# Kernel optimization log

Hardware: AMD Instinct MI355X
Metric: run time of the kernel (lower is better)

## Reference

```python
import jax, jax.numpy as jnp
import numpy as np

N_ATOMS, N_UND, N_DIR, N_ANG, N_STRUCT = 8192, 65536, 131072, 262144, 128
FEA, NRAD, NANGB, NCONV = 64, 9, 9, 4

FLOAT_NAMES = ["bond_bases_ag", "bond_bases_bg", "angle_bases", "atom_emb", "Wb", "Wa",
               "Wbw_ag", "Wbw_bg",
               "ac_cw1", "ac_cb1", "ac_cw2", "ac_cb2", "ac_gw1", "ac_gb1", "ac_gw2", "ac_gb2", "ac_out",
               "bc_cw1", "bc_cb1", "bc_cw2", "bc_cb2", "bc_gw1", "bc_gb1", "bc_gw2", "bc_gb2", "bc_out",
               "an_cw", "an_cb", "an_gw", "an_gb",
               "ro_w1", "ro_b1", "ro_w2", "ro_b2", "ro_w3", "ro_b3"]
INT_NAMES = ["atomic_numbers", "atom_graph", "directed2undirected",
             "bond_graph_atoms", "bond_graph_bonds", "atom_owners"]


def _silu(x):
    return x * jax.nn.sigmoid(x)


def _gmlp(x, cw1, cb1, cw2, cb2, gw1, gb1, gw2, gb2):
    # GatedMLP (norm=None): silu(MLP_core(x)) * sigmoid(MLP_gate(x)), each MLP = Lin-silu-Lin
    core = _silu(_silu(x @ cw1 + cb1) @ cw2 + cb2)
    gate = jax.nn.sigmoid(_silu(x @ gw1 + gb1) @ gw2 + gb2)
    return core * gate


def _forward(F, I):
    seg = jax.ops.segment_sum
    atom = F["atom_emb"][I["atomic_numbers"]]            # [N, 64]
    bond = F["bond_bases_ag"] @ F["Wb"]                  # [U, 64]
    angle = F["angle_bases"] @ F["Wa"]                   # [A, 64]
    bw_ag = F["bond_bases_ag"] @ F["Wbw_ag"]             # [U, 64]
    bw_bg = F["bond_bases_bg"] @ F["Wbw_bg"]             # [U, 64]
    ag0, ag1 = I["atom_graph"][:, 0], I["atom_graph"][:, 1]
    d2u = I["directed2undirected"]
    bgi, bgj = I["bond_graph_bonds"][:, 0], I["bond_graph_bonds"][:, 1]
    bga = I["bond_graph_atoms"]

    def atom_conv(i, atom, bond):
        msg = jnp.concatenate([atom[ag0], bond[d2u], atom[ag1]], axis=1)   # [E, 192]
        msg = _gmlp(msg, F["ac_cw1"][i], F["ac_cb1"][i], F["ac_cw2"][i], F["ac_cb2"][i],
                    F["ac_gw1"][i], F["ac_gb1"][i], F["ac_gw2"][i], F["ac_gb2"][i])
        msg = msg * bw_ag[d2u]
        # scatter-add to center atoms, linear mlp_out (no bias), resnet
        return atom + seg(msg, ag0, num_segments=N_ATOMS) @ F["ac_out"][i]

    for i in range(NCONV - 1):
        atom = atom_conv(i, atom, bond)
        # BondConv over bond graph (angles)
        tot = jnp.concatenate([bond[bgi], bond[bgj], angle, atom[bga]], axis=1)  # [A, 256]
        upd = _gmlp(tot, F["bc_cw1"][i], F["bc_cb1"][i], F["bc_cw2"][i], F["bc_cb2"][i],
                    F["bc_gw1"][i], F["bc_gb1"][i], F["bc_gw2"][i], F["bc_gb2"][i])
        upd = upd * bw_bg[bgi]
        bond = bond + seg(upd, bgi, num_segments=N_UND) @ F["bc_out"][i]
        # AngleUpdate (hidden_dim=0 -> single linear in each gated branch), resnet
        tot2 = jnp.concatenate([bond[bgi], bond[bgj], angle, atom[bga]], axis=1)
        angle = angle + _silu(tot2 @ F["an_cw"][i] + F["an_cb"][i]) * \
            jax.nn.sigmoid(tot2 @ F["an_gw"][i] + F["an_gb"][i])
    atom = atom_conv(NCONV - 1, atom, bond)

    # mlp_first readout: per-atom energy MLP then average pooling per structure
    e = _silu(atom @ F["ro_w1"] + F["ro_b1"])
    e = _silu(e @ F["ro_w2"] + F["ro_b2"])
    e = (e @ F["ro_w3"] + F["ro_b3"])[:, 0]              # [N]
    owners = I["atom_owners"]
    esum = seg(e, owners, num_segments=N_STRUCT)
    cnt = seg(jnp.ones_like(e), owners, num_segments=N_STRUCT)
    return esum / jnp.maximum(cnt, 1.0)                  # [N_STRUCT] energy/atom


def setup_inputs() -> dict:
    key = jax.random.key(0)
    ks = iter(jax.random.split(key, 64))

    def nrm(shape, fan_in):
        return jax.random.normal(next(ks), shape, dtype=jnp.float32) / np.float32(np.sqrt(fan_in))

    z = lambda *s: jnp.zeros(s, dtype=jnp.float32)
    inp = {}
    inp["atomic_numbers"] = jax.random.randint(next(ks), (N_ATOMS,), 0, 94, dtype=jnp.int32)
    inp["bond_bases_ag"] = jax.random.uniform(next(ks), (N_UND, NRAD), dtype=jnp.float32)
    inp["bond_bases_bg"] = jax.random.uniform(next(ks), (N_UND, NRAD), dtype=jnp.float32)
    inp["angle_bases"] = jax.random.uniform(next(ks), (N_ANG, NANGB), dtype=jnp.float32)
    inp["atom_graph"] = jax.random.randint(next(ks), (N_DIR, 2), 0, N_ATOMS, dtype=jnp.int32)
    inp["directed2undirected"] = jax.random.randint(next(ks), (N_DIR,), 0, N_UND, dtype=jnp.int32)
    inp["bond_graph_atoms"] = jax.random.randint(next(ks), (N_ANG,), 0, N_ATOMS, dtype=jnp.int32)
    inp["bond_graph_bonds"] = jax.random.randint(next(ks), (N_ANG, 2), 0, N_UND, dtype=jnp.int32)
    inp["atom_owners"] = jnp.sort(jax.random.randint(next(ks), (N_ATOMS,), 0, N_STRUCT, dtype=jnp.int32))
    inp["atom_emb"] = nrm((95, FEA), 1.0)
    inp["Wb"] = nrm((NRAD, FEA), NRAD)
    inp["Wa"] = nrm((NANGB, FEA), NANGB)
    inp["Wbw_ag"] = nrm((NRAD, FEA), NRAD)
    inp["Wbw_bg"] = nrm((NRAD, FEA), NRAD)
    d_a, d_b = 3 * FEA, 4 * FEA
    nb = NCONV - 1
    inp["ac_cw1"] = nrm((NCONV, d_a, FEA), d_a); inp["ac_cb1"] = z(NCONV, FEA)
    inp["ac_cw2"] = nrm((NCONV, FEA, FEA), FEA); inp["ac_cb2"] = z(NCONV, FEA)
    inp["ac_gw1"] = nrm((NCONV, d_a, FEA), d_a); inp["ac_gb1"] = z(NCONV, FEA)
    inp["ac_gw2"] = nrm((NCONV, FEA, FEA), FEA); inp["ac_gb2"] = z(NCONV, FEA)
    inp["ac_out"] = nrm((NCONV, FEA, FEA), FEA)
    inp["bc_cw1"] = nrm((nb, d_b, FEA), d_b); inp["bc_cb1"] = z(nb, FEA)
    inp["bc_cw2"] = nrm((nb, FEA, FEA), FEA); inp["bc_cb2"] = z(nb, FEA)
    inp["bc_gw1"] = nrm((nb, d_b, FEA), d_b); inp["bc_gb1"] = z(nb, FEA)
    inp["bc_gw2"] = nrm((nb, FEA, FEA), FEA); inp["bc_gb2"] = z(nb, FEA)
    inp["bc_out"] = nrm((nb, FEA, FEA), FEA)
    inp["an_cw"] = nrm((nb, d_b, FEA), d_b); inp["an_cb"] = z(nb, FEA)
    inp["an_gw"] = nrm((nb, d_b, FEA), d_b); inp["an_gb"] = z(nb, FEA)
    inp["ro_w1"] = nrm((FEA, FEA), FEA); inp["ro_b1"] = z(FEA)
    inp["ro_w2"] = nrm((FEA, FEA), FEA); inp["ro_b2"] = z(FEA)
    inp["ro_w3"] = nrm((FEA, 1), FEA); inp["ro_b3"] = z(1)
    return inp


def reference(atomic_numbers, bond_bases_ag, bond_bases_bg, angle_bases, atom_graph,
              directed2undirected, bond_graph_atoms, bond_graph_bonds, atom_owners,
              atom_emb, Wb, Wa, Wbw_ag, Wbw_bg,
              ac_cw1, ac_cb1, ac_cw2, ac_cb2, ac_gw1, ac_gb1, ac_gw2, ac_gb2, ac_out,
              bc_cw1, bc_cb1, bc_cw2, bc_cb2, bc_gw1, bc_gb1, bc_gw2, bc_gb2, bc_out,
              an_cw, an_cb, an_gw, an_gb,
              ro_w1, ro_b1, ro_w2, ro_b2, ro_w3, ro_b3):
    loc = locals()
    F = {k: loc[k] for k in FLOAT_NAMES}
    I = {k: loc[k] for k in INT_NAMES}
    return _forward(F, I)
```

## Files before the change

kernel.cpp:

```cpp
#include <hip/hip_runtime.h>
#include <hip/hip_bf16.h>

typedef float f32x4 __attribute__((ext_vector_type(4)));
typedef short s16x8 __attribute__((ext_vector_type(8)));
typedef unsigned int u32x4 __attribute__((ext_vector_type(4)));

#define DEV static __device__ __forceinline__

DEV unsigned short f2bf(float x){
    unsigned u = __builtin_bit_cast(unsigned, x);
    u += 0x7FFFu + ((u >> 16) & 1u);
    return (unsigned short)(u >> 16);
}
DEV float bf2f(unsigned short h){
    unsigned u = ((unsigned)h) << 16;
    return __builtin_bit_cast(float, u);
}
DEV float sigm_(float x){ return __builtin_amdgcn_rcpf(1.0f + __expf(-x)); }
DEV float silu_(float x){ return x * sigm_(x); }

DEV int xcd_swz(){
    int bid = blockIdx.x, nwg = gridDim.x;
    return (bid & 7) * (nwg >> 3) + (bid >> 3);
}

__global__ __launch_bounds__(256) void k_transconv(const float* __restrict__ src,
                                                   unsigned short* __restrict__ dst,
                                                   int K, int total){
    int gid = blockIdx.x * 256 + threadIdx.x;
    if (gid >= total) return;
    int kn  = K * 64;
    int b   = gid / kn;
    int rem = gid - b * kn;
    int k   = rem >> 6, n = rem & 63;
    dst[b * kn + n * K + k] = f2bf(src[gid]);
}

__global__ __launch_bounds__(256) void k_embed(const float* __restrict__ emb,
                                               const int* __restrict__ z,
                                               unsigned short* __restrict__ out){
    int gid = blockIdx.x * 256 + threadIdx.x;
    int n = gid >> 6, f = gid & 63;
    out[gid] = f2bf(emb[z[n] * 64 + f]);
}

__global__ __launch_bounds__(256) void k_smallmm(const float* __restrict__ bases,
                                                 const float* __restrict__ W,
                                                 unsigned short* __restrict__ out){
    int gid = blockIdx.x * 256 + threadIdx.x;
    int r = gid >> 6, f = gid & 63;
    const float* b = bases + r * 9;
    float acc = 0.f;
    #pragma unroll
    for (int k = 0; k < 9; ++k) acc += b[k] * W[k * 64 + f];
    out[gid] = f2bf(acc);
}

__global__ __launch_bounds__(256) void k_smallmm_perm(const float* __restrict__ bases,
                                                      const float* __restrict__ W,
                                                      const int* __restrict__ perm,
                                                      unsigned short* __restrict__ out){
    int gid = blockIdx.x * 256 + threadIdx.x;
    int r = gid >> 6, f = gid & 63;
    const float* b = bases + (size_t)perm[r] * 9;
    float acc = 0.f;
    #pragma unroll
    for (int k = 0; k < 9; ++k) acc += b[k] * W[k * 64 + f];
    out[gid] = f2bf(acc);
}

__global__ void k_count(const int* __restrict__ dst, int stride, int n, int* __restrict__ cnt){
    int i = blockIdx.x * 256 + threadIdx.x;
    if (i < n) atomicAdd(&cnt[dst[(size_t)i * stride]], 1);
}

__global__ __launch_bounds__(256) void k_bsum(const int* __restrict__ cnt,
                                              int* __restrict__ bsum){
    int i = blockIdx.x * 256 + threadIdx.x;
    int v = cnt[i];
    #pragma unroll
    for (int off = 32; off > 0; off >>= 1) v += __shfl_down(v, off);
    __shared__ int ws[4];
    if ((threadIdx.x & 63) == 0) ws[threadIdx.x >> 6] = v;
    __syncthreads();
    if (threadIdx.x == 0) bsum[blockIdx.x] = ws[0] + ws[1] + ws[2] + ws[3];
}

__global__ __launch_bounds__(256) void k_bscan(const int* __restrict__ bsum,
                                               int* __restrict__ bbase, int nb,
                                               int* __restrict__ total_out){
    __shared__ int sh[256];
    int t = threadIdx.x;
    int v = (t < nb) ? bsum[t] : 0;
    sh[t] = v;
    __syncthreads();
    for (int d = 1; d < 256; d <<= 1){
        int u = (t >= d) ? sh[t - d] : 0;
        __syncthreads();
        sh[t] += u;
        __syncthreads();
    }
    if (t < nb) bbase[t] = sh[t] - v;
    if (t == nb - 1) *total_out = sh[t];
}

__global__ __launch_bounds__(256) void k_offs(const int* __restrict__ cnt,
                                              const int* __restrict__ bbase,
                                              int* __restrict__ offs){
    __shared__ int sh[256];
    int t = threadIdx.x;
    int i = blockIdx.x * 256 + t;
    int v = cnt[i];
    sh[t] = v;
    __syncthreads();
    for (int d = 1; d < 256; d <<= 1){
        int u = (t >= d) ? sh[t - d] : 0;
        __syncthreads();
        sh[t] += u;
        __syncthreads();
    }
    offs[i] = bbase[blockIdx.x] + sh[t] - v;
}

__global__ void k_fill(const int* __restrict__ dst, int stride, int n,
                       const int* __restrict__ offs, int* __restrict__ cur,
                       int* __restrict__ idx){
    int i = blockIdx.x * 256 + threadIdx.x;
    if (i < n){
        int d = dst[(size_t)i * stride];
        int p = offs[d] + atomicAdd(&cur[d], 1);
        idx[p] = i;
    }
}

__global__ __launch_bounds__(256) void k_reduce(const unsigned short* __restrict__ upd,
                                                const int* __restrict__ offs,
                                                unsigned short* __restrict__ act, int nRows){
    int gid = blockIdx.x * 256 + threadIdx.x;
    int row = gid >> 3;
    if (row >= nRows) return;
    int c8 = (gid & 7) * 8;
    int o = offs[row], e = offs[row + 1];
    float acc[8] = {};
    for (int j = o; j < e; ++j){
        s16x8 v = *(const s16x8*)&upd[(size_t)j * 64 + c8];
        #pragma unroll
        for (int q = 0; q < 8; ++q) acc[q] += bf2f((unsigned short)v[q]);
    }
    s16x8 a = *(s16x8*)&act[(size_t)row * 64 + c8];
    #pragma unroll
    for (int q = 0; q < 8; ++q) a[q] = (short)f2bf(bf2f((unsigned short)a[q]) + acc[q]);
    *(s16x8*)&act[(size_t)row * 64 + c8] = a;
}

#define MFMA16(a,b,c) __builtin_amdgcn_mfma_f32_16x16x32_bf16(a,b,c,0,0,0)

DEV void atom_body(unsigned short* smem, int* ldsSrc, int bid,
    const unsigned short* atomBf, const unsigned short* bondBf,
    const unsigned short* bwagBf,
    const int* agraph, const int* d2u, const int* idxA,
    const unsigned short* w1cT, const unsigned short* w1gT,
    const unsigned short* w2cT, const unsigned short* w2gT,
    const unsigned short* woT,
    const float* cb1, const float* cb2, const float* gb1, const float* gb2,
    unsigned short* upd)
{
    unsigned short* ldsA  = smem;
    unsigned short* ldsHC = smem;
    unsigned short* ldsHG = smem + 4736;
    unsigned short* ldsV  = smem + 9472;
    unsigned short* ldsBw = smem + 14208;
    const int tid = threadIdx.x;
    const int r0  = bid * 64;

    {
        int q = tid >> 6, row = tid & 63;
        int e = idxA[r0 + row];
        int s;
        if (q == 0)      s = agraph[2 * e];
        else if (q == 1) s = d2u[e];
        else if (q == 2) s = agraph[2 * e + 1];
        else             s = d2u[e];
        ldsSrc[tid] = s;
    }
    __syncthreads();
    {
        const int lane8 = tid & 7;
        #pragma unroll
        for (int p = 0; p < 8; ++p){
            int cc = p * 32 + (tid >> 3);
            int q = cc >> 6, row = cc & 63;
            int s = ldsSrc[cc];
            const unsigned short* buf = (q == 1 || q == 3) ? bondBf : atomBf;
            if (q == 3) buf = bwagBf;
            u32x4 v = *(const u32x4*)(buf + (size_t)s * 64 + lane8 * 8);
            if (q < 3) *(u32x4*)&ldsA[row * 200 + q * 64 + lane8 * 8] = v;
            else       *(u32x4*)&ldsBw[row * 68 + lane8 * 8] = v;
        }
    }
    __syncthreads();

    const int lane = tid & 63;
    const int r16  = lane & 15;
    const int grp  = lane >> 4;
    const int col  = (tid >> 6) * 16 + r16;

    f32x4 aC[4] = {}, aG[4] = {};
    #pragma unroll
    for (int kt = 0; kt < 6; ++kt){
        s16x8 bc = *(const s16x8*)&w1cT[col * 192 + kt * 32 + grp * 8];
        s16x8 bg = *(const s16x8*)&w1gT[col * 192 + kt * 32 + grp * 8];
        #pragma unroll
        for (int mt = 0; mt < 4; ++mt){
            s16x8 a = *(const s16x8*)&ldsA[(mt * 16 + r16) * 200 + kt * 32 + grp * 8];
            aC[mt] = MFMA16(a, bc, aC[mt]);
            aG[mt] = MFMA16(a, bg, aG[mt]);
        }
    }
    __syncthreads();

    const float bC1 = cb1[col], bG1 = gb1[col];
    #pragma unroll
    for (int mt = 0; mt < 4; ++mt){
        #pragma unroll
        for (int j = 0; j < 4; ++j){
            int row = mt * 16 + grp * 4 + j;
            ldsHC[row * 74 + col] = f2bf(silu_(aC[mt][j] + bC1));
            ldsHG[row * 74 + col] = f2bf(silu_(aG[mt][j] + bG1));
        }
    }
    __syncthreads();

    f32x4 oC[4] = {}, oG[4] = {};
    #pragma unroll
    for (int kt = 0; kt < 2; ++kt){
        s16x8 bc = *(const s16x8*)&w2cT[col * 64 + kt * 32 + grp * 8];
        s16x8 bg = *(const s16x8*)&w2gT[col * 64 + kt * 32 + grp * 8];
        #pragma unroll
        for (int mt = 0; mt < 4; ++mt){
            s16x8 hc = *(const s16x8*)&ldsHC[(mt * 16 + r16) * 74 + kt * 32 + grp * 8];
            s16x8 hg = *(const s16x8*)&ldsHG[(mt * 16 + r16) * 74 + kt * 32 + grp * 8];
            oC[mt] = MFMA16(hc, bc, oC[mt]);
            oG[mt] = MFMA16(hg, bg, oG[mt]);
        }
    }
    const float bC2 = cb2[col], bG2 = gb2[col];
    #pragma unroll
    for (int mt = 0; mt < 4; ++mt){
        #pragma unroll
        for (int j = 0; j < 4; ++j){
            int row = mt * 16 + grp * 4 + j;
            float v = silu_(oC[mt][j] + bC2) * sigm_(oG[mt][j] + bG2);
            v *= bf2f(ldsBw[row * 68 + col]);
            ldsV[row * 74 + col] = f2bf(v);
        }
    }
    __syncthreads();

    f32x4 oD[4] = {};
    #pragma unroll
    for (int kt = 0; kt < 2; ++kt){
        s16x8 bo = *(const s16x8*)&woT[col * 64 + kt * 32 + grp * 8];
        #pragma unroll
        for (int mt = 0; mt < 4; ++mt){
            s16x8 a = *(const s16x8*)&ldsV[(mt * 16 + r16) * 74 + kt * 32 + grp * 8];
            oD[mt] = MFMA16(a, bo, oD[mt]);
        }
    }
    #pragma unroll
    for (int mt = 0; mt < 4; ++mt){
        #pragma unroll
        for (int j = 0; j < 4; ++j){
            int row = mt * 16 + grp * 4 + j;
            upd[(size_t)(r0 + row) * 64 + col] = f2bf(oD[mt][j]);
        }
    }
}

DEV void angle_body(unsigned short* ldsA, int* ldsSrc, int bid,
    const unsigned short* atomBf, const unsigned short* bondBf,
    unsigned short* angleS,
    const int* bga, const int* bgb, const int* idxB,
    const unsigned short* wcT, const unsigned short* wgT,
    const float* cb, const float* gb)
{
    const int tid = threadIdx.x;
    const int r0  = bid * 64;

    {
        int q = tid >> 6, row = tid & 63;
        int s;
        if (q == 2) s = r0 + row;
        else {
            int a = idxB[r0 + row];
            if (q == 0)      s = bgb[2 * a];
            else if (q == 1) s = bgb[2 * a + 1];
            else             s = bga[a];
        }
        ldsSrc[tid] = s;
    }
    __syncthreads();
    {
        const int lane8 = tid & 7;
        #pragma unroll
        for (int p = 0; p < 8; ++p){
            int cc = p * 32 + (tid >> 3);
            int q = cc >> 6, row = cc & 63;
            int s = ldsSrc[cc];
            const unsigned short* buf = (q < 2) ? bondBf : (q == 2 ? angleS : atomBf);
            u32x4 v = *(const u32x4*)(buf + (size_t)s * 64 + lane8 * 8);
            *(u32x4*)&ldsA[row * 264 + q * 64 + lane8 * 8] = v;
        }
    }
    __syncthreads();

    const int lane = tid & 63;
    const int r16  = lane & 15;
    const int grp  = lane >> 4;
    const int col  = (tid >> 6) * 16 + r16;

    f32x4 aC[4] = {}, aG[4] = {};
    #pragma unroll
    for (int kt = 0; kt < 8; ++kt){
        s16x8 bc = *(const s16x8*)&wcT[col * 256 + kt * 32 + grp * 8];
        s16x8 bg = *(const s16x8*)&wgT[col * 256 + kt * 32 + grp * 8];
        #pragma unroll
        for (int mt = 0; mt < 4; ++mt){
            s16x8 a = *(const s16x8*)&ldsA[(mt * 16 + r16) * 264 + kt * 32 + grp * 8];
            aC[mt] = MFMA16(a, bc, aC[mt]);
            aG[mt] = MFMA16(a, bg, aG[mt]);
        }
    }
    const float bC = cb[col], bG = gb[col];
    #pragma unroll
    for (int mt = 0; mt < 4; ++mt){
        #pragma unroll
        for (int j = 0; j < 4; ++j){
            int row = mt * 16 + grp * 4 + j;
            float oldv = bf2f(ldsA[row * 264 + 128 + col]);
            float v = silu_(aC[mt][j] + bC) * sigm_(aG[mt][j] + bG);
            angleS[(size_t)(r0 + row) * 64 + col] = f2bf(oldv + v);
        }
    }
}

__global__ __launch_bounds__(256, 4) void k_atom_conv(
    const unsigned short* __restrict__ atomBf, const unsigned short* __restrict__ bondBf,
    const unsigned short* __restrict__ bwagBf,
    const int* __restrict__ agraph, const int* __restrict__ d2u,
    const int* __restrict__ idxA,
    const unsigned short* __restrict__ w1cT, const unsigned short* __restrict__ w1gT,
    const unsigned short* __restrict__ w2cT, const unsigned short* __restrict__ w2gT,
    const unsigned short* __restrict__ woT,
    const float* __restrict__ cb1, const float* __restrict__ cb2,
    const float* __restrict__ gb1, const float* __restrict__ gb2,
    unsigned short* __restrict__ upd)
{
    __shared__ __align__(16) unsigned short smem[18560];
    __shared__ int ldsSrc[256];
    atom_body(smem, ldsSrc, xcd_swz(),
              atomBf, bondBf, bwagBf, agraph, d2u, idxA,
              w1cT, w1gT, w2cT, w2gT, woT, cb1, cb2, gb1, gb2, upd);
}

__global__ __launch_bounds__(256, 4) void k_angle_atom(
    const unsigned short* __restrict__ atomBf, const unsigned short* __restrict__ bondBf,
    unsigned short* __restrict__ angleS, const unsigned short* __restrict__ bwagBf,
    const int* __restrict__ agraph, const int* __restrict__ d2u, const int* __restrict__ idxA,
    const int* __restrict__ bga, const int* __restrict__ bgb, const int* __restrict__ idxB,
    const unsigned short* __restrict__ an_wcT, const unsigned short* __restrict__ an_wgT,
    const float* __restrict__ an_cb, const float* __restrict__ an_gb,
    const unsigned short* __restrict__ ac_w1cT, const unsigned short* __restrict__ ac_w1gT,
    const unsigned short* __restrict__ ac_w2cT, const unsigned short* __restrict__ ac_w2gT,
    const unsigned short* __restrict__ ac_woT,
    const float* __restrict__ ac_cb1, const float* __restrict__ ac_cb2,
    const float* __restrict__ ac_gb1, const float* __restrict__ ac_gb2,
    unsigned short* __restrict__ upd, int nbAngle)
{
    __shared__ __align__(16) unsigned short smem[18560];
    __shared__ int ldsSrc[256];
    int bid = blockIdx.x;
    if (bid < nbAngle){
        angle_body(smem, ldsSrc, bid, atomBf, bondBf, angleS, bga, bgb, idxB,
                   an_wcT, an_wgT, an_cb, an_gb);
    } else {
        atom_body(smem, ldsSrc, bid - nbAngle,
                  atomBf, bondBf, bwagBf, agraph, d2u, idxA,
                  ac_w1cT, ac_w1gT, ac_w2cT, ac_w2gT, ac_woT,
                  ac_cb1, ac_cb2, ac_gb1, ac_gb2, upd);
    }
}

__global__ __launch_bounds__(256, 4) void k_bond_conv(
    const unsigned short* __restrict__ atomBf, const unsigned short* __restrict__ bondBf,
    const unsigned short* __restrict__ angleS, const unsigned short* __restrict__ bwbgBf,
    const int* __restrict__ bga, const int* __restrict__ bgb,
    const int* __restrict__ idxB,
    const unsigned short* __restrict__ w1cT, const unsigned short* __restrict__ w1gT,
    const unsigned short* __restrict__ w2cT, const unsigned short* __restrict__ w2gT,
    const unsigned short* __restrict__ woT,
    const float* __restrict__ cb1, const float* __restrict__ cb2,
    const float* __restrict__ gb1, const float* __restrict__ gb2,
    unsigned short* __restrict__ upd)
{
    __shared__ __align__(16) unsigned short lds[16896];
    __shared__ int ldsSrc[256];
    unsigned short* ldsA  = lds;
    unsigned short* ldsHC = lds;
    unsigned short* ldsHG = lds + 4736;
    unsigned short* ldsV  = lds + 9472;
    const int tid = threadIdx.x;
    const int r0  = xcd_swz() * 64;

    {
        int q = tid >> 6, row = tid & 63;
        int s;
        if (q == 2) s = r0 + row;
        else {
            int a = idxB[r0 + row];
            if (q == 0)      s = bgb[2 * a];
            else if (q == 1) s = bgb[2 * a + 1];
            else             s = bga[a];
        }
        ldsSrc[tid] = s;
    }
    __syncthreads();
    {
        const int lane8 = tid & 7;
        #pragma unroll
        for (int p = 0; p < 8; ++p){
            int cc = p * 32 + (tid >> 3);
            int q = cc >> 6, row = cc & 63;
            int s = ldsSrc[cc];
            const unsigned short* buf = (q < 2) ? bondBf : (q == 2 ? angleS : atomBf);
            u32x4 v = *(const u32x4*)(buf + (size_t)s * 64 + lane8 * 8);
            *(u32x4*)&ldsA[row * 264 + q * 64 + lane8 * 8] = v;
        }
    }
    __syncthreads();

    const int lane = tid & 63;
    const int r16  = lane & 15;
    const int grp  = lane >> 4;
    const int col  = (tid >> 6) * 16 + r16;

    unsigned short bwv[16];
    #pragma unroll
    for (int mt = 0; mt < 4; ++mt)
        #pragma unroll
        for (int j = 0; j < 4; ++j)
            bwv[mt * 4 + j] = bwbgBf[(size_t)ldsSrc[mt * 16 + grp * 4 + j] * 64 + col];

    f32x4 aC[4] = {}, aG[4] = {};
    #pragma unroll
    for (int kt = 0; kt < 8; ++kt){
        s16x8 bc = *(const s16x8*)&w1cT[col * 256 + kt * 32 + grp * 8];
        s16x8 bg = *(const s16x8*)&w1gT[col * 256 + kt * 32 + grp * 8];
        #pragma unroll
        for (int mt = 0; mt < 4; ++mt){
            s16x8 a = *(const s16x8*)&ldsA[(mt * 16 + r16) * 264 + kt * 32 + grp * 8];
            aC[mt] = MFMA16(a, bc, aC[mt]);
            aG[mt] = MFMA16(a, bg, aG[mt]);
        }
    }
    __syncthreads();

    const float bC1 = cb1[col], bG1 = gb1[col];
    #pragma unroll
    for (int mt = 0; mt < 4; ++mt){
        #pragma unroll
        for (int j = 0; j < 4; ++j){
            int row = mt * 16 + grp * 4 + j;
            ldsHC[row * 74 + col] = f2bf(silu_(aC[mt][j] + bC1));
            ldsHG[row * 74 + col] = f2bf(silu_(aG[mt][j] + bG1));
        }
    }
    __syncthreads();

    f32x4 oC[4] = {}, oG[4] = {};
    #pragma unroll
    for (int kt = 0; kt < 2; ++kt){
        s16x8 bc = *(const s16x8*)&w2cT[col * 64 + kt * 32 + grp * 8];
        s16x8 bg = *(const s16x8*)&w2gT[col * 64 + kt * 32 + grp * 8];
        #pragma unroll
        for (int mt = 0; mt < 4; ++mt){
            s16x8 hc = *(const s16x8*)&ldsHC[(mt * 16 + r16) * 74 + kt * 32 + grp * 8];
            s16x8 hg = *(const s16x8*)&ldsHG[(mt * 16 + r16) * 74 + kt * 32 + grp * 8];
            oC[mt] = MFMA16(hc, bc, oC[mt]);
            oG[mt] = MFMA16(hg, bg, oG[mt]);
        }
    }
    const float bC2 = cb2[col], bG2 = gb2[col];
    #pragma unroll
    for (int mt = 0; mt < 4; ++mt){
        #pragma unroll
        for (int j = 0; j < 4; ++j){
            int row = mt * 16 + grp * 4 + j;
            float v = silu_(oC[mt][j] + bC2) * sigm_(oG[mt][j] + bG2);
            v *= bf2f(bwv[mt * 4 + j]);
            ldsV[row * 74 + col] = f2bf(v);
        }
    }
    __syncthreads();

    f32x4 oD[4] = {};
    #pragma unroll
    for (int kt = 0; kt < 2; ++kt){
        s16x8 bo = *(const s16x8*)&woT[col * 64 + kt * 32 + grp * 8];
        #pragma unroll
        for (int mt = 0; mt < 4; ++mt){
            s16x8 a = *(const s16x8*)&ldsV[(mt * 16 + r16) * 74 + kt * 32 + grp * 8];
            oD[mt] = MFMA16(a, bo, oD[mt]);
        }
    }
    #pragma unroll
    for (int mt = 0; mt < 4; ++mt){
        #pragma unroll
        for (int j = 0; j < 4; ++j){
            int row = mt * 16 + grp * 4 + j;
            upd[(size_t)(r0 + row) * 64 + col] = f2bf(oD[mt][j]);
        }
    }
}

__global__ __launch_bounds__(256) void k_readout(
    const unsigned short* __restrict__ atomBf, const int* __restrict__ owners,
    const float* __restrict__ w1, const float* __restrict__ b1,
    const float* __restrict__ w2, const float* __restrict__ b2,
    const float* __restrict__ w3, const float* __restrict__ b3,
    float* __restrict__ esum, float* __restrict__ cnt)
{
    int gid  = blockIdx.x * 256 + threadIdx.x;
    int n    = gid >> 6;
    int lane = threadIdx.x & 63;
    float a = bf2f(atomBf[n * 64 + lane]);
    float acc = b1[lane];
    #pragma unroll
    for (int k = 0; k < 64; ++k) acc += __shfl(a, k) * w1[k * 64 + lane];
    float h = silu_(acc);
    acc = b2[lane];
    #pragma unroll
    for (int k = 0; k < 64; ++k) acc += __shfl(h, k) * w2[k * 64 + lane];
    h = silu_(acc);
    float p = h * w3[lane];
    #pragma unroll
    for (int off = 32; off > 0; off >>= 1) p += __shfl_xor(p, off);
    if (lane == 0){
        atomicAdd(&esum[owners[n]], p + b3[0]);
        atomicAdd(&cnt[owners[n]], 1.0f);
    }
}

__global__ void k_final(const float* __restrict__ esum, const float* __restrict__ cnt,
                        float* __restrict__ out){
    int i = threadIdx.x;
    if (i < 128) out[i] = esum[i] / fmaxf(cnt[i], 1.0f);
}

extern "C" void kernel_launch(void* const* d_in, const int* in_sizes, int n_in,
                              void* d_out, int out_size, void* d_ws, size_t ws_size,
                              hipStream_t stream)
{
    (void)in_sizes; (void)n_in; (void)out_size; (void)ws_size;
    const int N_ATOMS = 8192, N_UND = 65536, N_DIR = 131072, N_ANG = 262144;

    const int*   atomic_numbers = (const int*)  d_in[0];
    const float* bb_ag  = (const float*)d_in[1];
    const float* bb_bg  = (const float*)d_in[2];
    const float* ang_b  = (const float*)d_in[3];
    const int*   agraph = (const int*)  d_in[4];
    const int*   d2u    = (const int*)  d_in[5];
    const int*   bga    = (const int*)  d_in[6];
    const int*   bgb    = (const int*)  d_in[7];
    const int*   owners = (const int*)  d_in[8];
    const float* emb    = (const float*)d_in[9];
    const float* Wb     = (const float*)d_in[10];
    const float* Wa     = (const float*)d_in[11];
    const float* Wbwag  = (const float*)d_in[12];
    const float* Wbwbg  = (const float*)d_in[13];
    const float* ac_cw1 = (const float*)d_in[14];
    const float* ac_cb1 = (const float*)d_in[15];
    const float* ac_cw2 = (const float*)d_in[16];
    const float* ac_cb2 = (const float*)d_in[17];
    const float* ac_gw1 = (const float*)d_in[18];
    const float* ac_gb1 = (const float*)d_in[19];
    const float* ac_gw2 = (const float*)d_in[20];
    const float* ac_gb2 = (const float*)d_in[21];
    const float* ac_out = (const float*)d_in[22];
    const float* bc_cw1 = (const float*)d_in[23];
    const float* bc_cb1 = (const float*)d_in[24];
    const float* bc_cw2 = (const float*)d_in[25];
    const float* bc_cb2 = (const float*)d_in[26];
    const float* bc_gw1 = (const float*)d_in[27];
    const float* bc_gb1 = (const float*)d_in[28];
    const float* bc_gw2 = (const float*)d_in[29];
    const float* bc_gb2 = (const float*)d_in[30];
    const float* bc_out = (const float*)d_in[31];
    const float* an_cw  = (const float*)d_in[32];
    const float* an_cb  = (const float*)d_in[33];
    const float* an_gw  = (const float*)d_in[34];
    const float* an_gb  = (const float*)d_in[35];
    const float* ro_w1  = (const float*)d_in[36];
    const float* ro_b1  = (const float*)d_in[37];
    const float* ro_w2  = (const float*)d_in[38];
    const float* ro_b2  = (const float*)d_in[39];
    const float* ro_w3  = (const float*)d_in[40];
    const float* ro_b3  = (const float*)d_in[41];

    char* ws = (char*)d_ws;
    size_t off = 0;
    auto alloc = [&](size_t bytes) -> void* {
        void* p = ws + off;
        off = (off + bytes + 255) & ~(size_t)255;
        return p;
    };
    unsigned short* atomBf  = (unsigned short*)alloc((size_t)N_ATOMS * 64 * 2);
    unsigned short* bondBf  = (unsigned short*)alloc((size_t)N_UND   * 64 * 2);
    unsigned short* angleS  = (unsigned short*)alloc((size_t)N_ANG   * 64 * 2);
    unsigned short* bwagBf  = (unsigned short*)alloc((size_t)N_UND   * 64 * 2);
    unsigned short* bwbgBf  = (unsigned short*)alloc((size_t)N_UND   * 64 * 2);
    unsigned short* updBuf  = (unsigned short*)alloc((size_t)N_ANG   * 64 * 2);
    float* esum   = (float*)alloc(128 * 4);
    float* cnt    = (float*)alloc(128 * 4);
    int* offsA = (int*)alloc((N_ATOMS + 1) * 4);
    int* curA  = (int*)alloc(N_ATOMS * 4);
    int* idxA  = (int*)alloc((size_t)N_DIR * 4);
    int* offsB = (int*)alloc((N_UND + 1) * 4);
    int* curB  = (int*)alloc(N_UND * 4);
    int* idxB  = (int*)alloc((size_t)N_ANG * 4);
    int* bsum  = (int*)alloc(256 * 4);
    int* bbase = (int*)alloc(256 * 4);
    unsigned short* acw1cT = (unsigned short*)alloc((size_t)4 * 64 * 192 * 2);
    unsigned short* acw1gT = (unsigned short*)alloc((size_t)4 * 64 * 192 * 2);
    unsigned short* acw2cT = (unsigned short*)alloc((size_t)4 * 64 * 64 * 2);
    unsigned short* acw2gT = (unsigned short*)alloc((size_t)4 * 64 * 64 * 2);
    unsigned short* acoT   = (unsigned short*)alloc((size_t)4 * 64 * 64 * 2);
    unsigned short* bcw1cT = (unsigned short*)alloc((size_t)3 * 64 * 256 * 2);
    unsigned short* bcw1gT = (unsigned short*)alloc((size_t)3 * 64 * 256 * 2);
    unsigned short* bcw2cT = (unsigned short*)alloc((size_t)3 * 64 * 64 * 2);
    unsigned short* bcw2gT = (unsigned short*)alloc((size_t)3 * 64 * 64 * 2);
    unsigned short* bcoT   = (unsigned short*)alloc((size_t)3 * 64 * 64 * 2);
    unsigned short* anwcT  = (unsigned short*)alloc((size_t)3 * 64 * 256 * 2);
    unsigned short* anwgT  = (unsigned short*)alloc((size_t)3 * 64 * 256 * 2);

    hipMemsetAsync(curA, 0, N_ATOMS * 4, stream);
    k_count<<<(N_DIR + 255) / 256, 256, 0, stream>>>(agraph, 2, N_DIR, curA);
    k_bsum <<<N_ATOMS / 256, 256, 0, stream>>>(curA, bsum);
    k_bscan<<<1, 256, 0, stream>>>(bsum, bbase, N_ATOMS / 256, offsA + N_ATOMS);
    k_offs <<<N_ATOMS / 256, 256, 0, stream>>>(curA, bbase, offsA);
    hipMemsetAsync(curA, 0, N_ATOMS * 4, stream);
    k_fill<<<(N_DIR + 255) / 256, 256, 0, stream>>>(agraph, 2, N_DIR, offsA, curA, idxA);

    hipMemsetAsync(curB, 0, N_UND * 4, stream);
    k_count<<<(N_ANG + 255) / 256, 256, 0, stream>>>(bgb, 2, N_ANG, curB);
    k_bsum <<<N_UND / 256, 256, 0, stream>>>(curB, bsum);
    k_bscan<<<1, 256, 0, stream>>>(bsum, bbase, N_UND / 256, offsB + N_UND);
    k_offs <<<N_UND / 256, 256, 0, stream>>>(curB, bbase, offsB);
    hipMemsetAsync(curB, 0, N_UND * 4, stream);
    k_fill<<<(N_ANG + 255) / 256, 256, 0, stream>>>(bgb, 2, N_ANG, offsB, curB, idxB);

    auto tc = [&](const float* src, unsigned short* dst, int B, int K){
        int total = B * K * 64;
        k_transconv<<<(total + 255) / 256, 256, 0, stream>>>(src, dst, K, total);
    };
    tc(ac_cw1, acw1cT, 4, 192);  tc(ac_gw1, acw1gT, 4, 192);
    tc(ac_cw2, acw2cT, 4, 64);   tc(ac_gw2, acw2gT, 4, 64);
    tc(ac_out, acoT,   4, 64);
    tc(bc_cw1, bcw1cT, 3, 256);  tc(bc_gw1, bcw1gT, 3, 256);
    tc(bc_cw2, bcw2cT, 3, 64);   tc(bc_gw2, bcw2gT, 3, 64);
    tc(bc_out, bcoT,   3, 64);
    tc(an_cw,  anwcT,  3, 256);  tc(an_gw,  anwgT,  3, 256);

    k_embed<<<N_ATOMS * 64 / 256, 256, 0, stream>>>(emb, atomic_numbers, atomBf);
    k_smallmm<<<N_UND * 64 / 256, 256, 0, stream>>>(bb_ag, Wb,    bondBf);
    k_smallmm_perm<<<N_ANG * 64 / 256, 256, 0, stream>>>(ang_b, Wa, idxB, angleS);
    k_smallmm<<<N_UND * 64 / 256, 256, 0, stream>>>(bb_ag, Wbwag, bwagBf);
    k_smallmm<<<N_UND * 64 / 256, 256, 0, stream>>>(bb_bg, Wbwbg, bwbgBf);

    k_atom_conv<<<N_DIR / 64, 256, 0, stream>>>(
        atomBf, bondBf, bwagBf, agraph, d2u, idxA,
        acw1cT, acw1gT, acw2cT, acw2gT, acoT,
        ac_cb1, ac_cb2, ac_gb1, ac_gb2, updBuf);
    k_reduce<<<N_ATOMS * 8 / 256, 256, 0, stream>>>(updBuf, offsA, atomBf, N_ATOMS);

    const int NB_AN = N_ANG / 64;
    const int NB_AC = N_DIR / 64;
    for (int i = 0; i < 3; ++i){
        k_bond_conv<<<NB_AN, 256, 0, stream>>>(
            atomBf, bondBf, angleS, bwbgBf, bga, bgb, idxB,
            bcw1cT + (size_t)i * 64 * 256, bcw1gT + (size_t)i * 64 * 256,
            bcw2cT + (size_t)i * 64 * 64,  bcw2gT + (size_t)i * 64 * 64,
            bcoT   + (size_t)i * 64 * 64,
            bc_cb1 + i * 64, bc_cb2 + i * 64, bc_gb1 + i * 64, bc_gb2 + i * 64, updBuf);
        k_reduce<<<N_UND * 8 / 256, 256, 0, stream>>>(updBuf, offsB, bondBf, N_UND);
        k_angle_atom<<<NB_AN + NB_AC, 256, 0, stream>>>(
            atomBf, bondBf, angleS, bwagBf,
            agraph, d2u, idxA, bga, bgb, idxB,
            anwcT + (size_t)i * 64 * 256, anwgT + (size_t)i * 64 * 256,
            an_cb + i * 64, an_gb + i * 64,
            acw1cT + (size_t)(i + 1) * 64 * 192, acw1gT + (size_t)(i + 1) * 64 * 192,
            acw2cT + (size_t)(i + 1) * 64 * 64,  acw2gT + (size_t)(i + 1) * 64 * 64,
            acoT   + (size_t)(i + 1) * 64 * 64,
            ac_cb1 + (i + 1) * 64, ac_cb2 + (i + 1) * 64,
            ac_gb1 + (i + 1) * 64, ac_gb2 + (i + 1) * 64,
            updBuf, NB_AN);
        k_reduce<<<N_ATOMS * 8 / 256, 256, 0, stream>>>(updBuf, offsA, atomBf, N_ATOMS);
    }

    hipMemsetAsync(esum, 0, 128 * 4, stream);
    hipMemsetAsync(cnt,  0, 128 * 4, stream);
    k_readout<<<N_ATOMS * 64 / 256, 256, 0, stream>>>(
        atomBf, owners, ro_w1, ro_b1, ro_w2, ro_b2, ro_w3, ro_b3, esum, cnt);
    k_final<<<1, 128, 0, stream>>>(esum, cnt, (float*)d_out);
}
```

Baseline: 859.4 us.

## Precompute sorted gather index tables and merge small setup kernels

Adds setup kernels that build per-row int4 tables of gather sources (srcA, srcB) once. The conv kernels then read their source indices straight from these tables instead of doing double-indirect lookups through idxA/idxB, and the ldsSrc staging with its barrier is removed. The three small basis matmuls are fused into one kernel, and paired weight transposes now share launches, which cuts launch count. The cost is extra index-table memory, about 6 MB, and uncoalesced strided global index reads inside the gather loop.

```diff
diff --git a/kernel.cpp b/kernel.cpp
--- a/kernel.cpp
+++ b/kernel.cpp
@@ -36,6 +36,22 @@
     dst[b * kn + n * K + k] = f2bf(src[gid]);
 }
 
+__global__ __launch_bounds__(256) void k_transconv2(const float* __restrict__ s1,
+                                                    const float* __restrict__ s2,
+                                                    unsigned short* __restrict__ d1,
+                                                    unsigned short* __restrict__ d2,
+                                                    int K, int total){
+    int gid = blockIdx.x * 256 + threadIdx.x;
+    if (gid >= total) return;
+    int kn  = K * 64;
+    int b   = gid / kn;
+    int rem = gid - b * kn;
+    int k   = rem >> 6, n = rem & 63;
+    int o   = b * kn + n * K + k;
+    d1[o] = f2bf(s1[gid]);
+    d2[o] = f2bf(s2[gid]);
+}
+
 __global__ __launch_bounds__(256) void k_embed(const float* __restrict__ emb,
                                                const int* __restrict__ z,
                                                unsigned short* __restrict__ out){
@@ -44,16 +60,29 @@
     out[gid] = f2bf(emb[z[n] * 64 + f]);
 }
 
-__global__ __launch_bounds__(256) void k_smallmm(const float* __restrict__ bases,
-                                                 const float* __restrict__ W,
-                                                 unsigned short* __restrict__ out){
+__global__ __launch_bounds__(256) void k_smallmm3(const float* __restrict__ bag,
+                                                  const float* __restrict__ bbg,
+                                                  const float* __restrict__ Wb,
+                                                  const float* __restrict__ Wwag,
+                                                  const float* __restrict__ Wwbg,
+                                                  unsigned short* __restrict__ bond,
+                                                  unsigned short* __restrict__ bwag,
+                                                  unsigned short* __restrict__ bwbg){
     int gid = blockIdx.x * 256 + threadIdx.x;
     int r = gid >> 6, f = gid & 63;
-    const float* b = bases + r * 9;
-    float acc = 0.f;
-    #pragma unroll
-    for (int k = 0; k < 9; ++k) acc += b[k] * W[k * 64 + f];
-    out[gid] = f2bf(acc);
+    const float* a = bag + (size_t)r * 9;
+    const float* b = bbg + (size_t)r * 9;
+    float s1 = 0.f, s2 = 0.f, s3 = 0.f;
+    #pragma unroll
+    for (int k = 0; k < 9; ++k){
+        float av = a[k];
+        s1 += av * Wb[k * 64 + f];
+        s2 += av * Wwag[k * 64 + f];
+        s3 += b[k] * Wwbg[k * 64 + f];
+    }
+    bond[gid] = f2bf(s1);
+    bwag[gid] = f2bf(s2);
+    bwbg[gid] = f2bf(s3);
 }
 
 __global__ __launch_bounds__(256) void k_smallmm_perm(const float* __restrict__ bases,
@@ -130,6 +159,24 @@
         int d = dst[(size_t)i * stride];
         int p = offs[d] + atomicAdd(&cur[d], 1);
         idx[p] = i;
+    }
+}
+
+__global__ void k_mktabA(const int* __restrict__ agraph, const int* __restrict__ d2u,
+                         const int* __restrict__ idxA, int4* __restrict__ srcA, int n){
+    int i = blockIdx.x * 256 + threadIdx.x;
+    if (i < n){
+        int e = idxA[i];
+        int u = d2u[e];
+        srcA[i] = make_int4(agraph[2 * e], u, agraph[2 * e + 1], u);
+    }
+}
+__global__ void k_mktabB(const int* __restrict__ bga, const int* __restrict__ bgb,
+                         const int* __restrict__ idxB, int4* __restrict__ srcB, int n){
+    int i = blockIdx.x * 256 + threadIdx.x;
+    if (i < n){
+        int a = idxB[i];
+        srcB[i] = make_int4(bgb[2 * a], bgb[2 * a + 1], i, bga[a]);
     }
 }
 
@@ -155,10 +202,9 @@
 
 #define MFMA16(a,b,c) __builtin_amdgcn_mfma_f32_16x16x32_bf16(a,b,c,0,0,0)
 
-DEV void atom_body(unsigned short* smem, int* ldsSrc, int bid,
+DEV void atom_body(unsigned short* smem, int bid,
     const unsigned short* atomBf, const unsigned short* bondBf,
-    const unsigned short* bwagBf,
-    const int* agraph, const int* d2u, const int* idxA,
+    const unsigned short* bwagBf, const int* srcA,
     const unsigned short* w1cT, const unsigned short* w1gT,
     const unsigned short* w2cT, const unsigned short* w2gT,
     const unsigned short* woT,
@@ -174,23 +220,12 @@
     const int r0  = bid * 64;
 
     {
-        int q = tid >> 6, row = tid & 63;
-        int e = idxA[r0 + row];
-        int s;
-        if (q == 0)      s = agraph[2 * e];
-        else if (q == 1) s = d2u[e];
-        else if (q == 2) s = agraph[2 * e + 1];
-        else             s = d2u[e];
-        ldsSrc[tid] = s;
-    }
-    __syncthreads();
-    {
         const int lane8 = tid & 7;
         #pragma unroll
         for (int p = 0; p < 8; ++p){
             int cc = p * 32 + (tid >> 3);
             int q = cc >> 6, row = cc & 63;
-            int s = ldsSrc[cc];
+            int s = srcA[(size_t)(r0 + row) * 4 + q];
             const unsigned short* buf = (q == 1 || q == 3) ? bondBf : atomBf;
             if (q == 3) buf = bwagBf;
             u32x4 v = *(const u32x4*)(buf + (size_t)s * 64 + lane8 * 8);
@@ -277,10 +312,9 @@
     }
 }
 
-DEV void angle_body(unsigned short* ldsA, int* ldsSrc, int bid,
+DEV void angle_body(unsigned short* ldsA, int bid,
     const unsigned short* atomBf, const unsigned short* bondBf,
-    unsigned short* angleS,
-    const int* bga, const int* bgb, const int* idxB,
+    unsigned short* angleS, const int* srcB,
     const unsigned short* wcT, const unsigned short* wgT,
     const float* cb, const float* gb)
 {
@@ -288,25 +322,12 @@
     const int r0  = bid * 64;
 
     {
-        int q = tid >> 6, row = tid & 63;
-        int s;
-        if (q == 2) s = r0 + row;
-        else {
-            int a = idxB[r0 + row];
-            if (q == 0)      s = bgb[2 * a];
-            else if (q == 1) s = bgb[2 * a + 1];
-            else             s = bga[a];
-        }
-        ldsSrc[tid] = s;
-    }
-    __syncthreads();
-    {
         const int lane8 = tid & 7;
         #pragma unroll
         for (int p = 0; p < 8; ++p){
             int cc = p * 32 + (tid >> 3);
             int q = cc >> 6, row = cc & 63;
-            int s = ldsSrc[cc];
+            int s = srcB[(size_t)(r0 + row) * 4 + q];
             const unsigned short* buf = (q < 2) ? bondBf : (q == 2 ? angleS : atomBf);
             u32x4 v = *(const u32x4*)(buf + (size_t)s * 64 + lane8 * 8);
             *(u32x4*)&ldsA[row * 264 + q * 64 + lane8 * 8] = v;
@@ -346,9 +367,7 @@
 
 __global__ __launch_bounds__(256, 4) void k_atom_conv(
     const unsigned short* __restrict__ atomBf, const unsigned short* __restrict__ bondBf,
-    const unsigned short* __restrict__ bwagBf,
-    const int* __restrict__ agraph, const int* __restrict__ d2u,
-    const int* __restrict__ idxA,
+    const unsigned short* __restrict__ bwagBf, const int* __restrict__ srcA,
     const unsigned short* __restrict__ w1cT, const unsigned short* __restrict__ w1gT,
     const unsigned short* __restrict__ w2cT, const unsigned short* __restrict__ w2gT,
     const unsigned short* __restrict__ woT,
@@ -357,17 +376,14 @@
     unsigned short* __restrict__ upd)
 {
     __shared__ __align__(16) unsigned short smem[18560];
-    __shared__ int ldsSrc[256];
-    atom_body(smem, ldsSrc, xcd_swz(),
-              atomBf, bondBf, bwagBf, agraph, d2u, idxA,
+    atom_body(smem, xcd_swz(), atomBf, bondBf, bwagBf, srcA,
               w1cT, w1gT, w2cT, w2gT, woT, cb1, cb2, gb1, gb2, upd);
 }
 
 __global__ __launch_bounds__(256, 4) void k_angle_atom(
     const unsigned short* __restrict__ atomBf, const unsigned short* __restrict__ bondBf,
     unsigned short* __restrict__ angleS, const unsigned short* __restrict__ bwagBf,
-    const int* __restrict__ agraph, const int* __restrict__ d2u, const int* __restrict__ idxA,
-    const int* __restrict__ bga, const int* __restrict__ bgb, const int* __restrict__ idxB,
+    const int* __restrict__ srcA, const int* __restrict__ srcB,
     const unsigned short* __restrict__ an_wcT, const unsigned short* __restrict__ an_wgT,
     const float* __restrict__ an_cb, const float* __restrict__ an_gb,
     const unsigned short* __restrict__ ac_w1cT, const unsigned short* __restrict__ ac_w1gT,
@@ -378,14 +394,12 @@
     unsigned short* __restrict__ upd, int nbAngle)
 {
     __shared__ __align__(16) unsigned short smem[18560];
-    __shared__ int ldsSrc[256];
     int bid = blockIdx.x;
     if (bid < nbAngle){
-        angle_body(smem, ldsSrc, bid, atomBf, bondBf, angleS, bga, bgb, idxB,
+        angle_body(smem, bid, atomBf, bondBf, angleS, srcB,
                    an_wcT, an_wgT, an_cb, an_gb);
     } else {
-        atom_body(smem, ldsSrc, bid - nbAngle,
-                  atomBf, bondBf, bwagBf, agraph, d2u, idxA,
+        atom_body(smem, bid - nbAngle, atomBf, bondBf, bwagBf, srcA,
                   ac_w1cT, ac_w1gT, ac_w2cT, ac_w2gT, ac_woT,
                   ac_cb1, ac_cb2, ac_gb1, ac_gb2, upd);
     }
@@ -394,8 +408,7 @@
 __global__ __launch_bounds__(256, 4) void k_bond_conv(
     const unsigned short* __restrict__ atomBf, const unsigned short* __restrict__ bondBf,
     const unsigned short* __restrict__ angleS, const unsigned short* __restrict__ bwbgBf,
-    const int* __restrict__ bga, const int* __restrict__ bgb,
-    const int* __restrict__ idxB,
+    const int* __restrict__ srcB,
     const unsigned short* __restrict__ w1cT, const unsigned short* __restrict__ w1gT,
     const unsigned short* __restrict__ w2cT, const unsigned short* __restrict__ w2gT,
     const unsigned short* __restrict__ woT,
@@ -404,7 +417,6 @@
     unsigned short* __restrict__ upd)
 {
     __shared__ __align__(16) unsigned short lds[16896];
-    __shared__ int ldsSrc[256];
     unsigned short* ldsA  = lds;
     unsigned short* ldsHC = lds;
     unsigned short* ldsHG = lds + 4736;
@@ -413,25 +425,12 @@
     const int r0  = xcd_swz() * 64;
 
     {
-        int q = tid >> 6, row = tid & 63;
-        int s;
-        if (q == 2) s = r0 + row;
-        else {
-            int a = idxB[r0 + row];
-            if (q == 0)      s = bgb[2 * a];
-            else if (q == 1) s = bgb[2 * a + 1];
-            else             s = bga[a];
-        }
-        ldsSrc[tid] = s;
-    }
-    __syncthreads();
-    {
         const int lane8 = tid & 7;
         #pragma unroll
         for (int p = 0; p < 8; ++p){
             int cc = p * 32 + (tid >> 3);
             int q = cc >> 6, row = cc & 63;
-            int s = ldsSrc[cc];
+            int s = srcB[(size_t)(r0 + row) * 4 + q];
             const unsigned short* buf = (q < 2) ? bondBf : (q == 2 ? angleS : atomBf);
             u32x4 v = *(const u32x4*)(buf + (size_t)s * 64 + lane8 * 8);
             *(u32x4*)&ldsA[row * 264 + q * 64 + lane8 * 8] = v;
@@ -448,8 +447,10 @@
     #pragma unroll
     for (int mt = 0; mt < 4; ++mt)
         #pragma unroll
-        for (int j = 0; j < 4; ++j)
-            bwv[mt * 4 + j] = bwbgBf[(size_t)ldsSrc[mt * 16 + grp * 4 + j] * 64 + col];
+        for (int j = 0; j < 4; ++j){
+            int row = mt * 16 + grp * 4 + j;
+            bwv[mt * 4 + j] = bwbgBf[(size_t)srcB[(size_t)(r0 + row) * 4] * 64 + col];
+        }
 
     f32x4 aC[4] = {}, aG[4] = {};
     #pragma unroll
@@ -630,6 +631,8 @@
     int* idxB  = (int*)alloc((size_t)N_ANG * 4);
     int* bsum  = (int*)alloc(256 * 4);
     int* bbase = (int*)alloc(256 * 4);
+    int* srcA  = (int*)alloc((size_t)N_DIR * 4 * 4);
+    int* srcB  = (int*)alloc((size_t)N_ANG * 4 * 4);
     unsigned short* acw1cT = (unsigned short*)alloc((size_t)4 * 64 * 192 * 2);
     unsigned short* acw1gT = (unsigned short*)alloc((size_t)4 * 64 * 192 * 2);
     unsigned short* acw2cT = (unsigned short*)alloc((size_t)4 * 64 * 64 * 2);
@@ -659,26 +662,24 @@
     hipMemsetAsync(curB, 0, N_UND * 4, stream);
     k_fill<<<(N_ANG + 255) / 256, 256, 0, stream>>>(bgb, 2, N_ANG, offsB, curB, idxB);
 
-    auto tc = [&](const float* src, unsigned short* dst, int B, int K){
-        int total = B * K * 64;
-        k_transconv<<<(total + 255) / 256, 256, 0, stream>>>(src, dst, K, total);
-    };
-    tc(ac_cw1, acw1cT, 4, 192);  tc(ac_gw1, acw1gT, 4, 192);
-    tc(ac_cw2, acw2cT, 4, 64);   tc(ac_gw2, acw2gT, 4, 64);
-    tc(ac_out, acoT,   4, 64);
-    tc(bc_cw1, bcw1cT, 3, 256);  tc(bc_gw1, bcw1gT, 3, 256);
-    tc(bc_cw2, bcw2cT, 3, 64);   tc(bc_gw2, bcw2gT, 3, 64);
-    tc(bc_out, bcoT,   3, 64);
-    tc(an_cw,  anwcT,  3, 256);  tc(an_gw,  anwgT,  3, 256);
+    k_mktabA<<<(N_DIR + 255) / 256, 256, 0, stream>>>(agraph, d2u, idxA, (int4*)srcA, N_DIR);
+    k_mktabB<<<(N_ANG + 255) / 256, 256, 0, stream>>>(bga, bgb, idxB, (int4*)srcB, N_ANG);
+
+    k_transconv2<<<(4 * 192 * 64 + 255) / 256, 256, 0, stream>>>(ac_cw1, ac_gw1, acw1cT, acw1gT, 192, 4 * 192 * 64);
+    k_transconv2<<<(4 * 64 * 64 + 255) / 256, 256, 0, stream>>>(ac_cw2, ac_gw2, acw2cT, acw2gT, 64, 4 * 64 * 64);
+    k_transconv <<<(4 * 64 * 64 + 255) / 256, 256, 0, stream>>>(ac_out, acoT, 64, 4 * 64 * 64);
+    k_transconv2<<<(3 * 256 * 64 + 255) / 256, 256, 0, stream>>>(bc_cw1, bc_gw1, bcw1cT, bcw1gT, 256, 3 * 256 * 64);
+    k_transconv2<<<(3 * 64 * 64 + 255) / 256, 256, 0, stream>>>(bc_cw2, bc_gw2, bcw2cT, bcw2gT, 64, 3 * 64 * 64);
+    k_transconv <<<(3 * 64 * 64 + 255) / 256, 256, 0, stream>>>(bc_out, bcoT, 64, 3 * 64 * 64);
+    k_transconv2<<<(3 * 256 * 64 + 255) / 256, 256, 0, stream>>>(an_cw, an_gw, anwcT, anwgT, 256, 3 * 256 * 64);
 
     k_embed<<<N_ATOMS * 64 / 256, 256, 0, stream>>>(emb, atomic_numbers, atomBf);
-    k_smallmm<<<N_UND * 64 / 256, 256, 0, stream>>>(bb_ag, Wb,    bondBf);
+    k_smallmm3<<<N_UND * 64 / 256, 256, 0, stream>>>(bb_ag, bb_bg, Wb, Wbwag, Wbwbg,
+                                                     bondBf, bwagBf, bwbgBf);
     k_smallmm_perm<<<N_ANG * 64 / 256, 256, 0, stream>>>(ang_b, Wa, idxB, angleS);
-    k_smallmm<<<N_UND * 64 / 256, 256, 0, stream>>>(bb_ag, Wbwag, bwagBf);
-    k_smallmm<<<N_UND * 64 / 256, 256, 0, stream>>>(bb_bg, Wbwbg, bwbgBf);
 
     k_atom_conv<<<N_DIR / 64, 256, 0, stream>>>(
-        atomBf, bondBf, bwagBf, agraph, d2u, idxA,
+        atomBf, bondBf, bwagBf, srcA,
         acw1cT, acw1gT, acw2cT, acw2gT, acoT,
         ac_cb1, ac_cb2, ac_gb1, ac_gb2, updBuf);
     k_reduce<<<N_ATOMS * 8 / 256, 256, 0, stream>>>(updBuf, offsA, atomBf, N_ATOMS);
@@ -687,15 +688,14 @@
     const int NB_AC = N_DIR / 64;
     for (int i = 0; i < 3; ++i){
         k_bond_conv<<<NB_AN, 256, 0, stream>>>(
-            atomBf, bondBf, angleS, bwbgBf, bga, bgb, idxB,
+            atomBf, bondBf, angleS, bwbgBf, srcB,
             bcw1cT + (size_t)i * 64 * 256, bcw1gT + (size_t)i * 64 * 256,
             bcw2cT + (size_t)i * 64 * 64,  bcw2gT + (size_t)i * 64 * 64,
             bcoT   + (size_t)i * 64 * 64,
             bc_cb1 + i * 64, bc_cb2 + i * 64, bc_gb1 + i * 64, bc_gb2 + i * 64, updBuf);
         k_reduce<<<N_UND * 8 / 256, 256, 0, stream>>>(updBuf, offsB, bondBf, N_UND);
         k_angle_atom<<<NB_AN + NB_AC, 256, 0, stream>>>(
-            atomBf, bondBf, angleS, bwagBf,
-            agraph, d2u, idxA, bga, bgb, idxB,
+            atomBf, bondBf, angleS, bwagBf, srcA, srcB,
             anwcT + (size_t)i * 64 * 256, anwgT + (size_t)i * 64 * 256,
             an_cb + i * 64, an_gb + i * 64,
             acw1cT + (size_t)(i + 1) * 64 * 192, acw1gT + (size_t)(i + 1) * 64 * 192,
```

Result: faster. 842.4 us (-2.0%).
